# Performance work log

Hardware: AMD Instinct MI355X
Metric: run time of the kernel (lower is better)

## Reference

```python
import jax, jax.numpy as jnp
import numpy as np

DIM = 64
D_STATE = 64          # = d_inner // 2, required for consistency
D_CONV = 4
EXPAND = 2
D_INNER = EXPAND * DIM  # 128
BATCH = 2
SEQ = 2048


def setup_inputs() -> dict:
    key = jax.random.key(0)
    k0, k1, k2, k3, k4, k5 = jax.random.split(key, 6)
    return {
        "x": jax.random.normal(k0, (BATCH, SEQ, DIM), jnp.float32),
        # torch nn.Linear weight layout: (out_features, in_features)
        "W_proj": jax.random.normal(k1, (3 * D_INNER, DIM), jnp.float32) / np.sqrt(DIM),
        # torch depthwise Conv1d weight layout: (d_inner, 1, d_conv)
        "conv_w": jax.random.normal(k2, (D_INNER, 1, D_CONV), jnp.float32) / np.sqrt(D_CONV),
        "conv_b": jax.random.normal(k3, (D_INNER,), jnp.float32) * 0.01,
        # negative A so exp(delta * rowsum(A)) is a stable decay (<1)
        "A": -jnp.abs(jax.random.normal(k4, (D_STATE, D_STATE), jnp.float32)) * 0.1,
        "D": jax.random.normal(k5, (D_INNER,), jnp.float32),
    }


def _scan_dir(A_bar, bx, reverse):
    # A_bar, bx: (B, L, n, d). Linear recurrence h_t = A_t * h_{t-1} + bx_t.
    A_t = jnp.moveaxis(A_bar, 1, 0)  # (L, B, n, d)
    b_t = jnp.moveaxis(bx, 1, 0)
    h0 = jnp.zeros(A_t.shape[1:], A_t.dtype)

    def step(h, inp):
        a, b = inp
        h = a * h + b
        return h, h

    _, hs = jax.lax.scan(step, h0, (A_t, b_t), reverse=reverse)
    return jnp.moveaxis(hs, 0, 1)  # (B, L, n, d)


def _forward(x, W_proj, conv_w, conv_b, A, D):
    d_inner = D.shape[0]
    n = A.shape[0]
    k = conv_w.shape[-1]

    xp = x @ W_proj.T                                   # (B, L, 3*d_inner)
    x_c_in, delta_raw, BC = jnp.split(xp, [d_inner, 2 * d_inner], axis=-1)

    # causal depthwise conv1d (torch pads d_conv-1 both sides then slices [:L])
    xc = jnp.swapaxes(x_c_in, 1, 2)                     # (B, d, L)
    xc = jax.lax.conv_general_dilated(
        xc, conv_w, window_strides=(1,), padding=[(k - 1, 0)],
        dimension_numbers=("NCH", "OIH", "NCH"), feature_group_count=d_inner)
    xc = xc + conv_b[None, :, None]
    x_conv = jnp.swapaxes(xc, 1, 2)                     # (B, L, d_inner)

    delta = jax.nn.sigmoid(delta_raw)                   # (B, L, d_inner)
    B_in, C_in = BC[..., :n], BC[..., n:]               # (B, L, n) each

    a = A.sum(axis=1)                                   # 'ij->i' contraction, (n,)
    # A_bar[b,l,n,d] = exp(delta[b,l,d] * a[n])
    A_bar = jnp.exp(delta[:, :, None, :] * a[None, None, :, None])
    # (delta*B) * x, broadcast into (B, L, n, d)
    bx = (delta * x_conv)[:, :, None, :] * B_in[..., None]

    h = _scan_dir(A_bar, bx, False) + _scan_dir(A_bar, bx, True)  # (B,L,n,d)

    y = jnp.einsum("blnd,bln->bld", h, C_in) + D * x_conv
    return y


def reference(x, W_proj, conv_w, conv_b, A, D):
    return _forward(x, W_proj, conv_w, conv_b, A, D)
```

## Files before the change

### kernel.cpp

```cpp
#include <hip/hip_runtime.h>

#define BB   2
#define TT   2048
#define DIN  128
#define NS   64
#define CL   16
#define NC   128
#define NSUP 16
#define SUPW 8
#define L2E  1.4426950408889634f

#if __has_builtin(__builtin_amdgcn_exp2f)
__device__ __forceinline__ float fexp2(float x) { return __builtin_amdgcn_exp2f(x); }
#else
__device__ __forceinline__ float fexp2(float x) { return exp2f(x); }
#endif

__global__ __launch_bounds__(128) void k_proj(
    const float* __restrict__ x, const float* __restrict__ W,
    const float* __restrict__ A,
    float* __restrict__ xcin, float* __restrict__ delta,
    float* __restrict__ Bb, float* __restrict__ Cb, float* __restrict__ a2g) {
  __shared__ float xs[128 * 65];
  int tile = blockIdx.x, rg = blockIdx.y, tid = threadIdx.x;
  int base = tile * 128;
  const float4* __restrict__ x4 = (const float4*)(x + (size_t)base * 64);
  for (int i = tid; i < 128 * 16; i += 128) {
    float4 v = x4[i];
    int row = i >> 4, c4 = (i & 15) << 2;
    xs[row * 65 + c4 + 0] = v.x;
    xs[row * 65 + c4 + 1] = v.y;
    xs[row * 65 + c4 + 2] = v.z;
    xs[row * 65 + c4 + 3] = v.w;
  }
  if (tile == 0 && rg == 0 && tid < NS) {
    float s = 0.f;
    for (int m = 0; m < NS; ++m) s += A[tid * NS + m];
    a2g[tid] = s * L2E;
  }
  __syncthreads();
  float xr[64];
#pragma unroll
  for (int k = 0; k < 64; ++k) xr[k] = xs[tid * 65 + k];
  int bt = base + tid;
#pragma unroll 4
  for (int rr = 0; rr < 16; ++rr) {
    int r = rg * 16 + rr;
    const float* __restrict__ wrow = W + r * 64;
    float a0 = 0.f, a1 = 0.f, a2 = 0.f, a3 = 0.f;
#pragma unroll
    for (int k = 0; k < 64; k += 4) {
      a0 = fmaf(xr[k + 0], wrow[k + 0], a0);
      a1 = fmaf(xr[k + 1], wrow[k + 1], a1);
      a2 = fmaf(xr[k + 2], wrow[k + 2], a2);
      a3 = fmaf(xr[k + 3], wrow[k + 3], a3);
    }
    float acc = (a0 + a1) + (a2 + a3);
    if (r < 128) {
      xcin[(size_t)bt * DIN + r] = acc;
    } else if (r < 256) {
      delta[(size_t)bt * DIN + (r - 128)] = 1.f / (1.f + fexp2(-acc * L2E));
    } else if (r < 320) {
      Bb[(size_t)bt * NS + (r - 256)] = acc;
    } else {
      Cb[(size_t)bt * NS + (r - 320)] = acc;
    }
  }
}

__global__ __launch_bounds__(1024) void k_scan1(
    const float* __restrict__ xcin, const float* __restrict__ delta,
    const float* __restrict__ Bb, const float* __restrict__ a2g,
    const float* __restrict__ cw, const float* __restrict__ cb,
    float* __restrict__ hend, float* __restrict__ sumd) {
  __shared__ float xcs[(CL + 3) * DIN];
  __shared__ float des[CL * DIN];
  __shared__ float Bs[CL * NS];
  int c = blockIdx.x, b = blockIdx.y;
  int tid = threadIdx.x;
  int d = tid & 127;
  int g = __builtin_amdgcn_readfirstlane(tid >> 7);
  int t0 = c * CL;
  {
    const float* __restrict__ xcB = xcin + (size_t)b * TT * DIN;
    for (int i = tid; i < (CL + 3) * 32; i += 1024) {
      int row = i >> 5, c4 = i & 31;
      int t = t0 - 3 + row;
      float4 v = make_float4(0.f, 0.f, 0.f, 0.f);
      if (t >= 0) v = ((const float4*)(xcB + (size_t)t * DIN))[c4];
      ((float4*)xcs)[i] = v;
    }
    if (tid < CL * 32)
      ((float4*)des)[tid] = ((const float4*)(delta + (size_t)(b * TT + t0) * DIN))[tid];
    if (tid < CL * 16)
      ((float4*)Bs)[tid] = ((const float4*)(Bb + (size_t)(b * TT + t0) * NS))[tid];
  }
  float cw0 = cw[d * 4 + 0], cw1 = cw[d * 4 + 1], cw2 = cw[d * 4 + 2], cw3 = cw[d * 4 + 3];
  float cbd = cb[d];
  int nb = g * 8;
  float a2r[8];
#pragma unroll
  for (int j = 0; j < 8; ++j) a2r[j] = a2g[nb + j];
  __syncthreads();
  float hf[8], hr[8], Pp[8];
#pragma unroll
  for (int j = 0; j < 8; ++j) { hf[j] = 0.f; hr[j] = 0.f; Pp[j] = 1.f; }
  float sd = 0.f;
  float w0 = xcs[0 * DIN + d], w1 = xcs[1 * DIN + d], w2 = xcs[2 * DIN + d];
#pragma unroll
  for (int i = 0; i < CL; ++i) {
    float w3 = xcs[(i + 3) * DIN + d];
    float xconv = fmaf(cw0, w0, fmaf(cw1, w1, fmaf(cw2, w2, fmaf(cw3, w3, cbd))));
    float de = des[i * DIN + d];
    sd += de;
    float dxv = de * xconv;
#pragma unroll
    for (int jq = 0; jq < 2; ++jq) {
      float4 bq = *(const float4*)&Bs[i * NS + nb + jq * 4];
      float b0 = dxv * bq.x, b1 = dxv * bq.y, b2 = dxv * bq.z, b3 = dxv * bq.w;
      float e0 = fexp2(de * a2r[jq * 4 + 0]);
      float e1 = fexp2(de * a2r[jq * 4 + 1]);
      float e2 = fexp2(de * a2r[jq * 4 + 2]);
      float e3 = fexp2(de * a2r[jq * 4 + 3]);
      hf[jq * 4 + 0] = fmaf(e0, hf[jq * 4 + 0], b0);
      hr[jq * 4 + 0] = fmaf(Pp[jq * 4 + 0], b0, hr[jq * 4 + 0]); Pp[jq * 4 + 0] *= e0;
      hf[jq * 4 + 1] = fmaf(e1, hf[jq * 4 + 1], b1);
      hr[jq * 4 + 1] = fmaf(Pp[jq * 4 + 1], b1, hr[jq * 4 + 1]); Pp[jq * 4 + 1] *= e1;
      hf[jq * 4 + 2] = fmaf(e2, hf[jq * 4 + 2], b2);
      hr[jq * 4 + 2] = fmaf(Pp[jq * 4 + 2], b2, hr[jq * 4 + 2]); Pp[jq * 4 + 2] *= e2;
      hf[jq * 4 + 3] = fmaf(e3, hf[jq * 4 + 3], b3);
      hr[jq * 4 + 3] = fmaf(Pp[jq * 4 + 3], b3, hr[jq * 4 + 3]); Pp[jq * 4 + 3] *= e3;
    }
    w0 = w1; w1 = w2; w2 = w3;
  }
  size_t h0 = (((size_t)(0 * NC + c) * BB + b) * NS + nb) * DIN + d;
  size_t h1 = (((size_t)(1 * NC + c) * BB + b) * NS + nb) * DIN + d;
#pragma unroll
  for (int j = 0; j < 8; ++j) {
    hend[h0 + (size_t)j * DIN] = hf[j];
    hend[h1 + (size_t)j * DIN] = hr[j];
  }
  if (g == 0) sumd[(c * BB + b) * DIN + d] = sd;
}

__global__ __launch_bounds__(512) void k_comb2A(
    const float* __restrict__ hend, float* __restrict__ hinL,
    const float* __restrict__ sumd, const float* __restrict__ a2g,
    float* __restrict__ S, float* __restrict__ sumdS,
    float* __restrict__ sumdPf, float* __restrict__ sumdPr) {
  int idx = blockIdx.x * 512 + threadIdx.x;
  int dd = idx & 127;
  int n = (idx >> 7) & 63;
  int sp = (idx >> 13) & 15;
  int bd = idx >> 17;
  int b = bd >> 1, dir = bd & 1;
  float a2n = a2g[n];
  float carry = 0.f;
  float running = 0.f;
#pragma unroll
  for (int k = 0; k < SUPW; ++k) {
    int cc = sp * SUPW + (dir ? (SUPW - 1 - k) : k);
    float sdv = sumd[(cc * BB + b) * DIN + dd];
    if (n == 0) {
      if (dir) sumdPr[(cc * BB + b) * DIN + dd] = running;
      else     sumdPf[(cc * BB + b) * DIN + dd] = running;
      running += sdv;
      if (dir == 0 && k == SUPW - 1) sumdS[(sp * BB + b) * DIN + dd] = running;
    }
    float e = fexp2(a2n * sdv);
    size_t hb = (((size_t)(dir * NC + cc) * BB + b) * NS + n) * DIN + dd;
    float tmp = hend[hb];
    hinL[hb] = carry;
    carry = fmaf(e, carry, tmp);
  }
  S[((((size_t)dir * NSUP + sp) * BB + b) * NS + n) * DIN + dd] = carry;
}

__global__ __launch_bounds__(256) void k_comb2B(
    const float* __restrict__ S, const float* __restrict__ sumdS,
    const float* __restrict__ a2g, float* __restrict__ Csup) {
  int idx = blockIdx.x * 256 + threadIdx.x;
  int dd = idx & 127;
  int n = (idx >> 7) & 63;
  int bd = idx >> 13;
  int b = bd >> 1, dir = bd & 1;
  float a2n = a2g[n];
  float sdS[NSUP], Sv[NSUP];
#pragma unroll
  for (int sp = 0; sp < NSUP; ++sp) {
    sdS[sp] = sumdS[(sp * BB + b) * DIN + dd];
    Sv[sp] = S[((((size_t)dir * NSUP + sp) * BB + b) * NS + n) * DIN + dd];
  }
  float carry = 0.f;
#pragma unroll
  for (int k = 0; k < NSUP; ++k) {
    int sp = dir ? (NSUP - 1 - k) : k;
    Csup[((((size_t)dir * NSUP + sp) * BB + b) * NS + n) * DIN + dd] = carry;
    carry = fmaf(fexp2(a2n * sdS[sp]), carry, Sv[sp]);
  }
}

__global__ __launch_bounds__(1024) void k_scan2(
    const float* __restrict__ xcin, const float* __restrict__ delta,
    const float* __restrict__ Bb, const float* __restrict__ Cb,
    const float* __restrict__ a2g, const float* __restrict__ cw,
    const float* __restrict__ cb, const float* __restrict__ Dp,
    const float* __restrict__ hinL, const float* __restrict__ Csup,
    const float* __restrict__ sumdPf, const float* __restrict__ sumdPr,
    float* __restrict__ out) {
  __shared__ float yred[8][CL][DIN];
  int c = blockIdx.x, b = blockIdx.y;
  int tid = threadIdx.x;
  int d = tid & 127;
  int g = __builtin_amdgcn_readfirstlane(tid >> 7);
  int dir = g >> 2;
  int nb = (g & 3) * 16;
  float cw0 = cw[d * 4 + 0], cw1 = cw[d * 4 + 1], cw2 = cw[d * 4 + 2], cw3 = cw[d * 4 + 3];
  float cbd = cb[d];
  float Dd = Dp[d];
  float a2r[16];
#pragma unroll
  for (int j = 0; j < 16; ++j) a2r[j] = a2g[nb + j];
  int sp = c >> 3;
  float Sloc = dir ? sumdPr[(c * BB + b) * DIN + d] : sumdPf[(c * BB + b) * DIN + d];
  float h[16];
  size_t hb0 = (((size_t)(dir * NC + c) * BB + b) * NS + nb) * DIN + d;
  size_t sb0 = ((((size_t)dir * NSUP + sp) * BB + b) * NS + nb) * DIN + d;
#pragma unroll
  for (int j = 0; j < 16; ++j) {
    float pe = fexp2(a2r[j] * Sloc);
    h[j] = fmaf(pe, Csup[sb0 + (size_t)j * DIN], hinL[hb0 + (size_t)j * DIN]);
  }
  int t0 = c * CL;
  const float* __restrict__ xcB = xcin + (size_t)b * TT * DIN + d;
  const float* __restrict__ deB = delta + (size_t)b * TT * DIN + d;
  const float* __restrict__ BbB = Bb + (size_t)b * TT * NS + nb;
  const float* __restrict__ CbB = Cb + (size_t)b * TT * NS + nb;
  bool addD = (g == 0);
  float w0, w1, w2, w3;
  if (dir == 0) {
    int t = t0;
    w0 = (t - 3 >= 0) ? xcB[(t - 3) * DIN] : 0.f;
    w1 = (t - 2 >= 0) ? xcB[(t - 2) * DIN] : 0.f;
    w2 = (t - 1 >= 0) ? xcB[(t - 1) * DIN] : 0.f;
    w3 = xcB[t * DIN];
#pragma unroll
    for (int i = 0; i < CL; ++i) {
      float xconv = fmaf(cw0, w0, fmaf(cw1, w1, fmaf(cw2, w2, fmaf(cw3, w3, cbd))));
      float de = deB[t * DIN];
      float dxv = de * xconv;
      float yv = addD ? Dd * xconv : 0.f;
#pragma unroll
      for (int jq = 0; jq < 4; ++jq) {
        float4 bq = *(const float4*)&BbB[t * NS + jq * 4];
        float4 cq = *(const float4*)&CbB[t * NS + jq * 4];
        float e0 = fexp2(de * a2r[jq * 4 + 0]);
        h[jq * 4 + 0] = fmaf(e0, h[jq * 4 + 0], dxv * bq.x); yv = fmaf(h[jq * 4 + 0], cq.x, yv);
        float e1 = fexp2(de * a2r[jq * 4 + 1]);
        h[jq * 4 + 1] = fmaf(e1, h[jq * 4 + 1], dxv * bq.y); yv = fmaf(h[jq * 4 + 1], cq.y, yv);
        float e2 = fexp2(de * a2r[jq * 4 + 2]);
        h[jq * 4 + 2] = fmaf(e2, h[jq * 4 + 2], dxv * bq.z); yv = fmaf(h[jq * 4 + 2], cq.z, yv);
        float e3 = fexp2(de * a2r[jq * 4 + 3]);
        h[jq * 4 + 3] = fmaf(e3, h[jq * 4 + 3], dxv * bq.w); yv = fmaf(h[jq * 4 + 3], cq.w, yv);
      }
      yred[g][i][d] = yv;
      if (i < CL - 1) { ++t; w0 = w1; w1 = w2; w2 = w3; w3 = xcB[t * DIN]; }
    }
  } else {
    int t = t0 + CL - 1;
    w3 = xcB[t * DIN];
    w2 = xcB[(t - 1) * DIN];
    w1 = xcB[(t - 2) * DIN];
    w0 = xcB[(t - 3) * DIN];
#pragma unroll
    for (int i = 0; i < CL; ++i) {
      float xconv = fmaf(cw0, w0, fmaf(cw1, w1, fmaf(cw2, w2, fmaf(cw3, w3, cbd))));
      float de = deB[t * DIN];
      float dxv = de * xconv;
      float yv = 0.f;
#pragma unroll
      for (int jq = 0; jq < 4; ++jq) {
        float4 bq = *(const float4*)&BbB[t * NS + jq * 4];
        float4 cq = *(const float4*)&CbB[t * NS + jq * 4];
        float e0 = fexp2(de * a2r[jq * 4 + 0]);
        h[jq * 4 + 0] = fmaf(e0, h[jq * 4 + 0], dxv * bq.x); yv = fmaf(h[jq * 4 + 0], cq.x, yv);
        float e1 = fexp2(de * a2r[jq * 4 + 1]);
        h[jq * 4 + 1] = fmaf(e1, h[jq * 4 + 1], dxv * bq.y); yv = fmaf(h[jq * 4 + 1], cq.y, yv);
        float e2 = fexp2(de * a2r[jq * 4 + 2]);
        h[jq * 4 + 2] = fmaf(e2, h[jq * 4 + 2], dxv * bq.z); yv = fmaf(h[jq * 4 + 2], cq.z, yv);
        float e3 = fexp2(de * a2r[jq * 4 + 3]);
        h[jq * 4 + 3] = fmaf(e3, h[jq * 4 + 3], dxv * bq.w); yv = fmaf(h[jq * 4 + 3], cq.w, yv);
      }
      yred[g][i][d] = yv;
      if (i < CL - 1) { --t; w3 = w2; w2 = w1; w1 = w0; w0 = (t - 3 >= 0) ? xcB[(t - 3) * DIN] : 0.f; }
    }
  }
  __syncthreads();
#pragma unroll
  for (int k = 0; k < 2; ++k) {
    int p = k * 1024 + tid;
    int i = p >> 7, d2 = p & 127;
    int ir = CL - 1 - i;
    float sf = (yred[0][i][d2] + yred[1][i][d2]) + (yred[2][i][d2] + yred[3][i][d2]);
    float sr = (yred[4][ir][d2] + yred[5][ir][d2]) + (yred[6][ir][d2] + yred[7][ir][d2]);
    out[((size_t)b * TT + t0 + i) * DIN + d2] = sf + sr;
  }
}

extern "C" void kernel_launch(void* const* d_in, const int* in_sizes, int n_in,
                              void* d_out, int out_size, void* d_ws, size_t ws_size,
                              hipStream_t stream) {
  const float* x  = (const float*)d_in[0];
  const float* W  = (const float*)d_in[1];
  const float* cw = (const float*)d_in[2];
  const float* cb = (const float*)d_in[3];
  const float* A  = (const float*)d_in[4];
  const float* Dp = (const float*)d_in[5];
  float* out = (float*)d_out;

  float* ws = (float*)d_ws;
  float* xcin   = ws;
  float* delta  = xcin + 524288;
  float* Bbuf   = delta + 524288;
  float* Cbuf   = Bbuf + 262144;
  float* a2g    = Cbuf + 262144;
  float* sumd   = a2g + 128;
  float* sumdPf = sumd + 32768;
  float* sumdPr = sumdPf + 32768;
  float* sumdS  = sumdPr + 32768;
  float* hendb  = sumdS + 4096;
  float* hinL   = hendb + 4194304;
  float* Sb     = hinL + 4194304;
  float* Csup   = Sb + 524288;

  hipLaunchKernelGGL(k_proj,   dim3(32, 24), dim3(128), 0, stream,
                     x, W, A, xcin, delta, Bbuf, Cbuf, a2g);
  hipLaunchKernelGGL(k_scan1,  dim3(NC, BB), dim3(1024), 0, stream,
                     xcin, delta, Bbuf, a2g, cw, cb, hendb, sumd);
  hipLaunchKernelGGL(k_comb2A, dim3(1024), dim3(512), 0, stream,
                     hendb, hinL, sumd, a2g, Sb, sumdS, sumdPf, sumdPr);
  hipLaunchKernelGGL(k_comb2B, dim3(128), dim3(256), 0, stream,
                     Sb, sumdS, a2g, Csup);
  hipLaunchKernelGGL(k_scan2,  dim3(NC, BB), dim3(1024), 0, stream,
                     xcin, delta, Bbuf, Cbuf, a2g, cw, cb, Dp, hinL, Csup,
                     sumdPf, sumdPr, out);
}
```

Baseline: 67.03 us.

## Fuse intra-superchunk combine into scan1 and store chunk carries as bf16

```diff
diff --git a/kernel.cpp b/kernel.cpp
--- a/kernel.cpp
+++ b/kernel.cpp
@@ -15,6 +15,15 @@
 #else
 __device__ __forceinline__ float fexp2(float x) { return exp2f(x); }
 #endif
+
+__device__ __forceinline__ unsigned short f2bf(float f) {
+  unsigned int u = __float_as_uint(f);
+  u += 0x7FFFu + ((u >> 16) & 1u);
+  return (unsigned short)(u >> 16);
+}
+__device__ __forceinline__ float bf2f(unsigned short s) {
+  return __uint_as_float(((unsigned int)s) << 16);
+}
 
 __global__ __launch_bounds__(128) void k_proj(
     const float* __restrict__ x, const float* __restrict__ W,
@@ -72,108 +81,110 @@
     const float* __restrict__ xcin, const float* __restrict__ delta,
     const float* __restrict__ Bb, const float* __restrict__ a2g,
     const float* __restrict__ cw, const float* __restrict__ cb,
-    float* __restrict__ hend, float* __restrict__ sumd) {
-  __shared__ float xcs[(CL + 3) * DIN];
-  __shared__ float des[CL * DIN];
-  __shared__ float Bs[CL * NS];
-  int c = blockIdx.x, b = blockIdx.y;
+    unsigned short* __restrict__ hinL, float* __restrict__ S,
+    float* __restrict__ sumd, float* __restrict__ sumdS,
+    float* __restrict__ sumdPf, float* __restrict__ sumdPr) {
+  __shared__ float Hs[SUPW][8][DIN];
+  __shared__ float sds[SUPW][DIN];
+  int bid = blockIdx.x;
+  int oct = bid >> 5;
+  int sb  = bid & 31;
+  int sp  = sb >> 1, b = sb & 1;
   int tid = threadIdx.x;
   int d = tid & 127;
   int g = __builtin_amdgcn_readfirstlane(tid >> 7);
+  int c = sp * SUPW + g;
   int t0 = c * CL;
-  {
-    const float* __restrict__ xcB = xcin + (size_t)b * TT * DIN;
-    for (int i = tid; i < (CL + 3) * 32; i += 1024) {
-      int row = i >> 5, c4 = i & 31;
-      int t = t0 - 3 + row;
-      float4 v = make_float4(0.f, 0.f, 0.f, 0.f);
-      if (t >= 0) v = ((const float4*)(xcB + (size_t)t * DIN))[c4];
-      ((float4*)xcs)[i] = v;
-    }
-    if (tid < CL * 32)
-      ((float4*)des)[tid] = ((const float4*)(delta + (size_t)(b * TT + t0) * DIN))[tid];
-    if (tid < CL * 16)
-      ((float4*)Bs)[tid] = ((const float4*)(Bb + (size_t)(b * TT + t0) * NS))[tid];
-  }
+  int nb = oct * 8;
+  float a2r[8];
+#pragma unroll
+  for (int j = 0; j < 8; ++j) a2r[j] = a2g[nb + j];
   float cw0 = cw[d * 4 + 0], cw1 = cw[d * 4 + 1], cw2 = cw[d * 4 + 2], cw3 = cw[d * 4 + 3];
   float cbd = cb[d];
-  int nb = g * 8;
-  float a2r[8];
-#pragma unroll
-  for (int j = 0; j < 8; ++j) a2r[j] = a2g[nb + j];
-  __syncthreads();
+  const float* __restrict__ xcB = xcin + (size_t)b * TT * DIN + d;
+  const float* __restrict__ deB = delta + (size_t)b * TT * DIN + d;
+  const float* __restrict__ BbB = Bb + (size_t)b * TT * NS + nb;
+
   float hf[8], hr[8], Pp[8];
 #pragma unroll
   for (int j = 0; j < 8; ++j) { hf[j] = 0.f; hr[j] = 0.f; Pp[j] = 1.f; }
   float sd = 0.f;
-  float w0 = xcs[0 * DIN + d], w1 = xcs[1 * DIN + d], w2 = xcs[2 * DIN + d];
+  float w0, w1, w2;
+  if (c == 0) { w0 = 0.f; w1 = 0.f; w2 = 0.f; }
+  else {
+    w0 = xcB[(t0 - 3) * DIN];
+    w1 = xcB[(t0 - 2) * DIN];
+    w2 = xcB[(t0 - 1) * DIN];
+  }
 #pragma unroll
   for (int i = 0; i < CL; ++i) {
-    float w3 = xcs[(i + 3) * DIN + d];
+    float w3 = xcB[(t0 + i) * DIN];
     float xconv = fmaf(cw0, w0, fmaf(cw1, w1, fmaf(cw2, w2, fmaf(cw3, w3, cbd))));
-    float de = des[i * DIN + d];
+    float de = deB[(t0 + i) * DIN];
     sd += de;
     float dxv = de * xconv;
-#pragma unroll
-    for (int jq = 0; jq < 2; ++jq) {
-      float4 bq = *(const float4*)&Bs[i * NS + nb + jq * 4];
-      float b0 = dxv * bq.x, b1 = dxv * bq.y, b2 = dxv * bq.z, b3 = dxv * bq.w;
-      float e0 = fexp2(de * a2r[jq * 4 + 0]);
-      float e1 = fexp2(de * a2r[jq * 4 + 1]);
-      float e2 = fexp2(de * a2r[jq * 4 + 2]);
-      float e3 = fexp2(de * a2r[jq * 4 + 3]);
-      hf[jq * 4 + 0] = fmaf(e0, hf[jq * 4 + 0], b0);
-      hr[jq * 4 + 0] = fmaf(Pp[jq * 4 + 0], b0, hr[jq * 4 + 0]); Pp[jq * 4 + 0] *= e0;
-      hf[jq * 4 + 1] = fmaf(e1, hf[jq * 4 + 1], b1);
-      hr[jq * 4 + 1] = fmaf(Pp[jq * 4 + 1], b1, hr[jq * 4 + 1]); Pp[jq * 4 + 1] *= e1;
-      hf[jq * 4 + 2] = fmaf(e2, hf[jq * 4 + 2], b2);
-      hr[jq * 4 + 2] = fmaf(Pp[jq * 4 + 2], b2, hr[jq * 4 + 2]); Pp[jq * 4 + 2] *= e2;
-      hf[jq * 4 + 3] = fmaf(e3, hf[jq * 4 + 3], b3);
-      hr[jq * 4 + 3] = fmaf(Pp[jq * 4 + 3], b3, hr[jq * 4 + 3]); Pp[jq * 4 + 3] *= e3;
+    float4 bq0 = *(const float4*)&BbB[(t0 + i) * NS];
+    float4 bq1 = *(const float4*)&BbB[(t0 + i) * NS + 4];
+    float bv[8] = {bq0.x, bq0.y, bq0.z, bq0.w, bq1.x, bq1.y, bq1.z, bq1.w};
+#pragma unroll
+    for (int j = 0; j < 8; ++j) {
+      float bj = dxv * bv[j];
+      float ej = fexp2(de * a2r[j]);
+      hf[j] = fmaf(ej, hf[j], bj);
+      hr[j] = fmaf(Pp[j], bj, hr[j]);
+      Pp[j] *= ej;
     }
     w0 = w1; w1 = w2; w2 = w3;
   }
-  size_t h0 = (((size_t)(0 * NC + c) * BB + b) * NS + nb) * DIN + d;
-  size_t h1 = (((size_t)(1 * NC + c) * BB + b) * NS + nb) * DIN + d;
-#pragma unroll
-  for (int j = 0; j < 8; ++j) {
-    hend[h0 + (size_t)j * DIN] = hf[j];
-    hend[h1 + (size_t)j * DIN] = hr[j];
-  }
-  if (g == 0) sumd[(c * BB + b) * DIN + d] = sd;
-}
-
-__global__ __launch_bounds__(512) void k_comb2A(
-    const float* __restrict__ hend, float* __restrict__ hinL,
-    const float* __restrict__ sumd, const float* __restrict__ a2g,
-    float* __restrict__ S, float* __restrict__ sumdS,
-    float* __restrict__ sumdPf, float* __restrict__ sumdPr) {
-  int idx = blockIdx.x * 512 + threadIdx.x;
-  int dd = idx & 127;
-  int n = (idx >> 7) & 63;
-  int sp = (idx >> 13) & 15;
-  int bd = idx >> 17;
-  int b = bd >> 1, dir = bd & 1;
-  float a2n = a2g[n];
-  float carry = 0.f;
-  float running = 0.f;
-#pragma unroll
-  for (int k = 0; k < SUPW; ++k) {
-    int cc = sp * SUPW + (dir ? (SUPW - 1 - k) : k);
-    float sdv = sumd[(cc * BB + b) * DIN + dd];
-    if (n == 0) {
-      if (dir) sumdPr[(cc * BB + b) * DIN + dd] = running;
-      else     sumdPf[(cc * BB + b) * DIN + dd] = running;
-      running += sdv;
-      if (dir == 0 && k == SUPW - 1) sumdS[(sp * BB + b) * DIN + dd] = running;
-    }
-    float e = fexp2(a2n * sdv);
-    size_t hb = (((size_t)(dir * NC + cc) * BB + b) * NS + n) * DIN + dd;
-    float tmp = hend[hb];
-    hinL[hb] = carry;
-    carry = fmaf(e, carry, tmp);
-  }
-  S[((((size_t)dir * NSUP + sp) * BB + b) * NS + n) * DIN + dd] = carry;
+  sds[g][d] = sd;
+#pragma unroll
+  for (int j = 0; j < 8; ++j) Hs[g][j][d] = hf[j];
+  __syncthreads();
+
+  if (oct == 0) {
+    float pf = 0.f, pr = 0.f;
+#pragma unroll
+    for (int k = 0; k < SUPW; ++k) {
+      float v = sds[k][d];
+      if (k < g) pf += v;
+      if (k > g) pr += v;
+    }
+    sumdPf[(c * BB + b) * DIN + d] = pf;
+    sumdPr[(c * BB + b) * DIN + d] = pr;
+    sumd[(c * BB + b) * DIN + d] = sds[g][d];
+    if (g == SUPW - 1) sumdS[(sp * BB + b) * DIN + d] = pf + sds[SUPW - 1][d];
+  }
+
+  float a2n = a2g[nb + g];
+  {
+    float carry = 0.f;
+#pragma unroll
+    for (int k = 0; k < SUPW; ++k) {
+      int cc = sp * SUPW + k;
+      float e = fexp2(a2n * sds[k][d]);
+      size_t hb = (((size_t)(0 * NC + cc) * BB + b) * NS + (nb + g)) * DIN + d;
+      hinL[hb] = f2bf(carry);
+      carry = fmaf(e, carry, Hs[k][g][d]);
+    }
+    S[(((size_t)(0 * NSUP + sp) * BB + b) * NS + (nb + g)) * DIN + d] = carry;
+  }
+  __syncthreads();
+#pragma unroll
+  for (int j = 0; j < 8; ++j) Hs[g][j][d] = hr[j];
+  __syncthreads();
+  {
+    float carry = 0.f;
+#pragma unroll
+    for (int kk = 0; kk < SUPW; ++kk) {
+      int k = SUPW - 1 - kk;
+      int cc = sp * SUPW + k;
+      float e = fexp2(a2n * sds[k][d]);
+      size_t hb = (((size_t)(1 * NC + cc) * BB + b) * NS + (nb + g)) * DIN + d;
+      hinL[hb] = f2bf(carry);
+      carry = fmaf(e, carry, Hs[k][g][d]);
+    }
+    S[(((size_t)(1 * NSUP + sp) * BB + b) * NS + (nb + g)) * DIN + d] = carry;
+  }
 }
 
 __global__ __launch_bounds__(256) void k_comb2B(
@@ -205,7 +216,7 @@
     const float* __restrict__ Bb, const float* __restrict__ Cb,
     const float* __restrict__ a2g, const float* __restrict__ cw,
     const float* __restrict__ cb, const float* __restrict__ Dp,
-    const float* __restrict__ hinL, const float* __restrict__ Csup,
+    const unsigned short* __restrict__ hinL, const float* __restrict__ Csup,
     const float* __restrict__ sumdPf, const float* __restrict__ sumdPr,
     float* __restrict__ out) {
   __shared__ float yred[8][CL][DIN];
@@ -229,7 +240,7 @@
 #pragma unroll
   for (int j = 0; j < 16; ++j) {
     float pe = fexp2(a2r[j] * Sloc);
-    h[j] = fmaf(pe, Csup[sb0 + (size_t)j * DIN], hinL[hb0 + (size_t)j * DIN]);
+    h[j] = fmaf(pe, Csup[sb0 + (size_t)j * DIN], bf2f(hinL[hb0 + (size_t)j * DIN]));
   }
   int t0 = c * CL;
   const float* __restrict__ xcB = xcin + (size_t)b * TT * DIN + d;
@@ -328,20 +339,18 @@
   float* sumdPf = sumd + 32768;
   float* sumdPr = sumdPf + 32768;
   float* sumdS  = sumdPr + 32768;
-  float* hendb  = sumdS + 4096;
-  float* hinL   = hendb + 4194304;
-  float* Sb     = hinL + 4194304;
+  float* Sb     = sumdS + 4096;
   float* Csup   = Sb + 524288;
+  unsigned short* hinLb = (unsigned short*)(Csup + 524288);
 
   hipLaunchKernelGGL(k_proj,   dim3(32, 24), dim3(128), 0, stream,
                      x, W, A, xcin, delta, Bbuf, Cbuf, a2g);
-  hipLaunchKernelGGL(k_scan1,  dim3(NC, BB), dim3(1024), 0, stream,
-                     xcin, delta, Bbuf, a2g, cw, cb, hendb, sumd);
-  hipLaunchKernelGGL(k_comb2A, dim3(1024), dim3(512), 0, stream,
-                     hendb, hinL, sumd, a2g, Sb, sumdS, sumdPf, sumdPr);
+  hipLaunchKernelGGL(k_scan1,  dim3(256), dim3(1024), 0, stream,
+                     xcin, delta, Bbuf, a2g, cw, cb, hinLb, Sb,
+                     sumd, sumdS, sumdPf, sumdPr);
   hipLaunchKernelGGL(k_comb2B, dim3(128), dim3(256), 0, stream,
                      Sb, sumdS, a2g, Csup);
   hipLaunchKernelGGL(k_scan2,  dim3(NC, BB), dim3(1024), 0, stream,
-                     xcin, delta, Bbuf, Cbuf, a2g, cw, cb, Dp, hinL, Csup,
+                     xcin, delta, Bbuf, Cbuf, a2g, cw, cb, Dp, hinLb, Csup,
                      sumdPf, sumdPr, out);
 }
```

New measurement: 102.1 us. +52.3%, slower.
